# Kernel optimization log

Hardware: AMD Instinct MI355X
Metric: run time of the kernel (lower is better)

Reference implementation:

```python
import jax, jax.numpy as jnp
import numpy as np

B, T, H, C = 32, 2048, 1024, 1024

def setup_inputs() -> dict:
    key = jax.random.key(0)
    k1, k2, k3, k4, k5, k6 = jax.random.split(key, 6)
    decoder_output = jax.random.normal(k1, (B, 1, H), dtype=jnp.float32)
    encoder_outputs = jax.random.normal(k2, (B, T, H), dtype=jnp.float32)
    scale = 1.0 / np.sqrt(H)
    W = jax.random.normal(k3, (H, C), dtype=jnp.float32) * scale
    V = jax.random.normal(k4, (H, C), dtype=jnp.float32) * scale
    b = jax.random.uniform(k5, (C,), dtype=jnp.float32, minval=-0.1, maxval=0.1)
    w = jax.random.normal(k6, (C, 1), dtype=jnp.float32) * (1.0 / np.sqrt(C))
    return {"decoder_output": decoder_output, "encoder_outputs": encoder_outputs,
            "W": W, "V": V, "b": b, "w": w}

def reference(decoder_output, encoder_outputs, W, V, b, w):
    # Additive (Bahdanau) content attention.
    dec_proj = jnp.einsum('bqh,hc->bqc', decoder_output, W)   # [B,1,C]
    enc_proj = jnp.einsum('bth,hc->btc', encoder_outputs, V)  # [B,T,C]
    energy = jnp.tanh(dec_proj + enc_proj + b)                # [B,T,C]
    scores = jnp.einsum('btc,c->bt', energy, w[:, 0])         # [B,T]
    alignment = jax.nn.softmax(scores, axis=-1)               # [B,T]
    context = jnp.einsum('bt,bth->bh', alignment, encoder_outputs)  # [B,H]
    return context
```

## Files before the change

### kernel.cpp

```cpp
#include <hip/hip_runtime.h>
#include <hip/hip_bf16.h>
#include <stdint.h>

#define Bn 32
#define Tn 2048
#define Hn 1024
#define Cn 1024

typedef short short8 __attribute__((ext_vector_type(8)));
typedef float floatx4 __attribute__((ext_vector_type(4)));

__device__ __forceinline__ unsigned int bf16_rne(float f) {
    union { float f; unsigned int u; } v; v.f = f;
    unsigned int u = v.u;
    return (u + 0x7fffu + ((u >> 16) & 1u)) >> 16;
}

__global__ void k_dbias(const float* __restrict__ dec, const float* __restrict__ W,
                        const float* __restrict__ bias, float* __restrict__ dbias) {
    const int b  = blockIdx.x;
    const int c  = blockIdx.y * 256 + threadIdx.x;
    const int h0 = blockIdx.z * 256;
    const float* dv = dec + b * Hn + h0;
    const float* wp = W + (size_t)h0 * Cn + c;
    float acc = 0.f;
#pragma unroll 8
    for (int h = 0; h < 256; ++h)
        acc += dv[h] * wp[(size_t)h * Cn];
    if (blockIdx.z == 0) acc += bias[c];
    atomicAdd(&dbias[b * Cn + c], acc);
}

__global__ void k_vpack(const float* __restrict__ V, uint4* __restrict__ vp) {
    const int bid  = blockIdx.x;
    const int nt   = bid >> 5;
    const int kt   = bid & 31;
    const int lane = threadIdx.x;
    const int c    = nt * 16 + (lane & 15);
    const int k0   = kt * 32 + (lane >> 4) * 8;
    unsigned int h[8];
#pragma unroll
    for (int j = 0; j < 8; ++j)
        h[j] = bf16_rne(V[(size_t)(k0 + j) * Cn + c]);
    uint4 u;
    u.x = h[0] | (h[1] << 16);
    u.y = h[2] | (h[3] << 16);
    u.z = h[4] | (h[5] << 16);
    u.w = h[6] | (h[7] << 16);
    vp[(size_t)bid * 64 + lane] = u;
}

#define BLK_M 64
#define LDA   1032

struct ScoresShared {
    unsigned short A[BLK_M * LDA];
    float scores[BLK_M];
};

__global__ __launch_bounds__(512, 2)
void k_scores(const float* __restrict__ enc, const uint4* __restrict__ vp,
              const float* __restrict__ dbias, const float* __restrict__ wv,
              float* __restrict__ scores_g) {
    __shared__ ScoresShared sh;
    const int wg   = blockIdx.x;
    const int tid  = threadIdx.x;
    const int lane = tid & 63;
    const int wave = tid >> 6;
    const int b    = wg >> 5;
    const int row0 = wg * BLK_M;
    const int lhi  = lane >> 4;
    const int llo  = lane & 15;

    if (tid < BLK_M) sh.scores[tid] = 0.f;

    {
        const float4* ep = (const float4*)(enc + (size_t)row0 * Hn);
#pragma unroll 4
        for (int it = 0; it < 32; ++it) {
            int idx = tid + it * 512;
            int r   = idx >> 8;
            int c4  = idx & 255;
            float4 f = ep[r * 256 + c4];
            uint2 p;
            p.x = bf16_rne(f.x) | (bf16_rne(f.y) << 16);
            p.y = bf16_rne(f.z) | (bf16_rne(f.w) << 16);
            *(uint2*)&sh.A[r * LDA + c4 * 4] = p;
        }
    }
    __syncthreads();

    float score_part[16];
#pragma unroll
    for (int i = 0; i < 16; ++i) score_part[i] = 0.f;

    for (int ni = 0; ni < 2; ++ni) {
        const int colbase = (ni * 8 + wave) * 64;
        const int nt0     = colbase >> 4;

        floatx4 acc[4][4];
#pragma unroll
        for (int i = 0; i < 4; ++i)
#pragma unroll
            for (int j = 0; j < 4; ++j)
                acc[i][j] = (floatx4){0.f, 0.f, 0.f, 0.f};

#pragma unroll 2
        for (int kt = 0; kt < 32; ++kt) {
            short8 afr[4], bfr[4];
#pragma unroll
            for (int rg = 0; rg < 4; ++rg) {
                const unsigned short* ap = &sh.A[(rg * 16 + llo) * LDA + kt * 32 + lhi * 8];
                afr[rg] = *(const short8*)ap;
            }
#pragma unroll
            for (int j = 0; j < 4; ++j) {
                uint4 u = vp[((nt0 + j) * 32 + kt) * 64 + lane];
                bfr[j] = __builtin_bit_cast(short8, u);
            }
#pragma unroll
            for (int rg = 0; rg < 4; ++rg)
#pragma unroll
                for (int j = 0; j < 4; ++j)
                    acc[rg][j] = __builtin_amdgcn_mfma_f32_16x16x32_bf16(
                        afr[rg], bfr[j], acc[rg][j], 0, 0, 0);
        }

#pragma unroll
        for (int j = 0; j < 4; ++j) {
            const int c  = colbase + j * 16 + llo;
            const float db = dbias[b * Cn + c];
            const float wc = wv[c];
#pragma unroll
            for (int rg = 0; rg < 4; ++rg) {
#pragma unroll
                for (int r = 0; r < 4; ++r) {
                    float x = acc[rg][j][r] + db;
                    x = fminf(fmaxf(x, -12.f), 12.f);
                    float e = __expf(2.f * x);
                    float t = 1.f - 2.f / (e + 1.f);
                    score_part[rg * 4 + r] += t * wc;
                }
            }
        }
    }

#pragma unroll
    for (int i = 0; i < 16; ++i) {
        float v = score_part[i];
        v += __shfl_xor(v, 1);
        v += __shfl_xor(v, 2);
        v += __shfl_xor(v, 4);
        v += __shfl_xor(v, 8);
        score_part[i] = v;
    }
    if (llo == 0) {
#pragma unroll
        for (int rg = 0; rg < 4; ++rg)
#pragma unroll
            for (int r = 0; r < 4; ++r)
                atomicAdd(&sh.scores[rg * 16 + lhi * 4 + r], score_part[rg * 4 + r]);
    }
    __syncthreads();
    if (tid < BLK_M) scores_g[row0 + tid] = sh.scores[tid];
}

__global__ void k_softmax(const float* __restrict__ scores, float* __restrict__ align) {
    const int b   = blockIdx.x;
    const int tid = threadIdx.x;
    const float* s = scores + b * Tn;
    float v[8];
    float lmax = -1e30f;
#pragma unroll
    for (int i = 0; i < 8; ++i) { v[i] = s[tid + i * 256]; lmax = fmaxf(lmax, v[i]); }
    for (int off = 1; off < 64; off <<= 1) lmax = fmaxf(lmax, __shfl_xor(lmax, off));
    __shared__ float red[4];
    __shared__ float red2[4];
    if ((tid & 63) == 0) red[tid >> 6] = lmax;
    __syncthreads();
    lmax = fmaxf(fmaxf(red[0], red[1]), fmaxf(red[2], red[3]));
    float lsum = 0.f;
#pragma unroll
    for (int i = 0; i < 8; ++i) { v[i] = __expf(v[i] - lmax); lsum += v[i]; }
    for (int off = 1; off < 64; off <<= 1) lsum += __shfl_xor(lsum, off);
    if ((tid & 63) == 0) red2[tid >> 6] = lsum;
    __syncthreads();
    lsum = red2[0] + red2[1] + red2[2] + red2[3];
    const float inv = 1.f / lsum;
#pragma unroll
    for (int i = 0; i < 8; ++i) align[b * Tn + tid + i * 256] = v[i] * inv;
}

__global__ void k_context(const float* __restrict__ enc, const float* __restrict__ align,
                          float* __restrict__ out) {
    const int b   = blockIdx.x;
    const int tc  = blockIdx.y;
    const int tid = threadIdx.x;
    const float4* ep = (const float4*)(enc + ((size_t)b * Tn + tc * 256) * Hn);
    const float*  al = align + b * Tn + tc * 256;
    float4 acc = {0.f, 0.f, 0.f, 0.f};
    for (int t = 0; t < 256; ++t) {
        const float a = al[t];
        const float4 e = ep[t * 256 + tid];
        acc.x += a * e.x; acc.y += a * e.y; acc.z += a * e.z; acc.w += a * e.w;
    }
    float* op = out + b * Hn + tid * 4;
    atomicAdd(op + 0, acc.x);
    atomicAdd(op + 1, acc.y);
    atomicAdd(op + 2, acc.z);
    atomicAdd(op + 3, acc.w);
}

extern "C" void kernel_launch(void* const* d_in, const int* in_sizes, int n_in,
                              void* d_out, int out_size, void* d_ws, size_t ws_size,
                              hipStream_t stream) {
    const float* dec  = (const float*)d_in[0];
    const float* enc  = (const float*)d_in[1];
    const float* W    = (const float*)d_in[2];
    const float* V    = (const float*)d_in[3];
    const float* bias = (const float*)d_in[4];
    const float* wv   = (const float*)d_in[5];
    float* out = (float*)d_out;

    char* ws = (char*)d_ws;
    float* dbias  = (float*)(ws);
    uint4* vpack  = (uint4*)(ws + 131072);
    float* scores = (float*)(ws + 131072 + 2097152);
    float* align  = (float*)(ws + 131072 + 2097152 + 262144);

    hipMemsetAsync(dbias, 0, 131072, stream);
    hipMemsetAsync(d_out, 0, Bn * Cn * sizeof(float), stream);

    k_dbias  <<<dim3(32, 4, 4), 256, 0, stream>>>(dec, W, bias, dbias);
    k_vpack  <<<2048, 64, 0, stream>>>(V, vpack);
    k_scores <<<1024, 512, 0, stream>>>(enc, vpack, dbias, wv, scores);
    k_softmax<<<32, 256, 0, stream>>>(scores, align);
    k_context<<<dim3(32, 8), 256, 0, stream>>>(enc, align, out);
}
```

Before: 569.5 us.

## Pipeline encoder tile loads via direct-to-LDS copies and split context into partial-reduce kernels

The scores kernel now streams the fp32 encoder tile into shared memory in four K-chunks, double-buffered with global_load_lds, and converts it to bf16 at fragment-load time. It also computes both N halves in one K pass, prefetching the packed V fragments one step ahead. This is meant to overlap global loads with MFMA work, at the cost of more registers and larger LDS traffic, since fp32 is stored instead of bf16. The context kernel is split into a 32-way T-partitioned partial pass with more parallelism and a separate reduction kernel, replacing atomics and the output memset.

```diff
diff --git a/kernel.cpp b/kernel.cpp
--- a/kernel.cpp
+++ b/kernel.cpp
@@ -14,6 +14,17 @@
     union { float f; unsigned int u; } v; v.f = f;
     unsigned int u = v.u;
     return (u + 0x7fffu + ((u >> 16) & 1u)) >> 16;
+}
+
+__device__ __forceinline__ unsigned int pk_bf16(float a, float b) {
+    return bf16_rne(a) | (bf16_rne(b) << 16);
+}
+
+__device__ __forceinline__ void load_lds_16(const float* g, float* l) {
+    __builtin_amdgcn_global_load_lds(
+        (const __attribute__((address_space(1))) unsigned int*)g,
+        (__attribute__((address_space(3))) unsigned int*)l,
+        16, 0, 0);
 }
 
 __global__ void k_dbias(const float* __restrict__ dec, const float* __restrict__ W,
@@ -51,10 +62,12 @@
 }
 
 #define BLK_M 64
-#define LDA   1032
+#define KC    256
+#define NCH   4
+#define LDAF  260
 
 struct ScoresShared {
-    unsigned short A[BLK_M * LDA];
+    float A[2][BLK_M][LDAF];
     float scores[BLK_M];
 };
 
@@ -63,10 +76,10 @@
               const float* __restrict__ dbias, const float* __restrict__ wv,
               float* __restrict__ scores_g) {
     __shared__ ScoresShared sh;
-    const int wg   = blockIdx.x;
     const int tid  = threadIdx.x;
     const int lane = tid & 63;
-    const int wave = tid >> 6;
+    const int wid  = tid >> 6;
+    const int wg   = blockIdx.x;
     const int b    = wg >> 5;
     const int row0 = wg * BLK_M;
     const int lhi  = lane >> 4;
@@ -74,68 +87,105 @@
 
     if (tid < BLK_M) sh.scores[tid] = 0.f;
 
-    {
-        const float4* ep = (const float4*)(enc + (size_t)row0 * Hn);
-#pragma unroll 4
-        for (int it = 0; it < 32; ++it) {
-            int idx = tid + it * 512;
-            int r   = idx >> 8;
-            int c4  = idx & 255;
-            float4 f = ep[r * 256 + c4];
-            uint2 p;
-            p.x = bf16_rne(f.x) | (bf16_rne(f.y) << 16);
-            p.y = bf16_rne(f.z) | (bf16_rne(f.w) << 16);
-            *(uint2*)&sh.A[r * LDA + c4 * 4] = p;
+    const float* grow = enc + (size_t)row0 * Hn + lane * 4;
+
+#pragma unroll
+    for (int i = 0; i < 8; ++i) {
+        const int r = wid * 8 + i;
+        load_lds_16(grow + (size_t)r * Hn, &sh.A[0][r][0]);
+    }
+    __syncthreads();
+
+    const int nt0 = wid * 4;
+    const int nt1 = (wid + 8) * 4;
+
+    floatx4 acc[2][4][4];
+#pragma unroll
+    for (int n = 0; n < 2; ++n)
+#pragma unroll
+        for (int i = 0; i < 4; ++i)
+#pragma unroll
+            for (int j = 0; j < 4; ++j)
+                acc[n][i][j] = (floatx4){0.f, 0.f, 0.f, 0.f};
+
+    for (int c = 0; c < NCH; ++c) {
+        const int cb = c & 1;
+        const int kbase = c * 8;
+
+        uint4 bcur[8];
+#pragma unroll
+        for (int j = 0; j < 4; ++j) {
+            bcur[j]     = vp[((nt0 + j) * 32 + kbase) * 64 + lane];
+            bcur[4 + j] = vp[((nt1 + j) * 32 + kbase) * 64 + lane];
         }
-    }
-    __syncthreads();
+
+#pragma unroll
+        for (int kt = 0; kt < 8; ++kt) {
+            uint4 bnxt[8];
+            if (kt < 7) {
+                const int kg = kbase + kt + 1;
+#pragma unroll
+                for (int j = 0; j < 4; ++j) {
+                    bnxt[j]     = vp[((nt0 + j) * 32 + kg) * 64 + lane];
+                    bnxt[4 + j] = vp[((nt1 + j) * 32 + kg) * 64 + lane];
+                }
+            }
+            if (c < NCH - 1 && kt < 4) {
+                const int r0 = wid * 8 + kt * 2;
+                const float* gsrc = grow + (size_t)(c + 1) * KC;
+                load_lds_16(gsrc + (size_t)r0 * Hn,       &sh.A[cb ^ 1][r0][0]);
+                load_lds_16(gsrc + (size_t)(r0 + 1) * Hn, &sh.A[cb ^ 1][r0 + 1][0]);
+            }
+
+            short8 afr[4];
+#pragma unroll
+            for (int rg = 0; rg < 4; ++rg) {
+                const float* ap = &sh.A[cb][rg * 16 + llo][kt * 32 + lhi * 8];
+                float4 f0 = *(const float4*)ap;
+                float4 f1 = *(const float4*)(ap + 4);
+                uint4 u;
+                u.x = pk_bf16(f0.x, f0.y);
+                u.y = pk_bf16(f0.z, f0.w);
+                u.z = pk_bf16(f1.x, f1.y);
+                u.w = pk_bf16(f1.z, f1.w);
+                afr[rg] = __builtin_bit_cast(short8, u);
+            }
+
+#pragma unroll
+            for (int rg = 0; rg < 4; ++rg)
+#pragma unroll
+                for (int j = 0; j < 4; ++j) {
+                    acc[0][rg][j] = __builtin_amdgcn_mfma_f32_16x16x32_bf16(
+                        afr[rg], __builtin_bit_cast(short8, bcur[j]), acc[0][rg][j], 0, 0, 0);
+                    acc[1][rg][j] = __builtin_amdgcn_mfma_f32_16x16x32_bf16(
+                        afr[rg], __builtin_bit_cast(short8, bcur[4 + j]), acc[1][rg][j], 0, 0, 0);
+                }
+
+            if (kt < 7) {
+#pragma unroll
+                for (int j = 0; j < 8; ++j) bcur[j] = bnxt[j];
+            }
+        }
+        __syncthreads();
+    }
 
     float score_part[16];
 #pragma unroll
     for (int i = 0; i < 16; ++i) score_part[i] = 0.f;
 
+#pragma unroll
     for (int ni = 0; ni < 2; ++ni) {
-        const int colbase = (ni * 8 + wave) * 64;
-        const int nt0     = colbase >> 4;
-
-        floatx4 acc[4][4];
-#pragma unroll
-        for (int i = 0; i < 4; ++i)
-#pragma unroll
-            for (int j = 0; j < 4; ++j)
-                acc[i][j] = (floatx4){0.f, 0.f, 0.f, 0.f};
-
-#pragma unroll 2
-        for (int kt = 0; kt < 32; ++kt) {
-            short8 afr[4], bfr[4];
+        const int colbase = (ni * 8 + wid) * 64;
+#pragma unroll
+        for (int j = 0; j < 4; ++j) {
+            const int cc   = colbase + j * 16 + llo;
+            const float db = dbias[b * Cn + cc];
+            const float wc = wv[cc];
 #pragma unroll
             for (int rg = 0; rg < 4; ++rg) {
-                const unsigned short* ap = &sh.A[(rg * 16 + llo) * LDA + kt * 32 + lhi * 8];
-                afr[rg] = *(const short8*)ap;
-            }
-#pragma unroll
-            for (int j = 0; j < 4; ++j) {
-                uint4 u = vp[((nt0 + j) * 32 + kt) * 64 + lane];
-                bfr[j] = __builtin_bit_cast(short8, u);
-            }
-#pragma unroll
-            for (int rg = 0; rg < 4; ++rg)
-#pragma unroll
-                for (int j = 0; j < 4; ++j)
-                    acc[rg][j] = __builtin_amdgcn_mfma_f32_16x16x32_bf16(
-                        afr[rg], bfr[j], acc[rg][j], 0, 0, 0);
-        }
-
-#pragma unroll
-        for (int j = 0; j < 4; ++j) {
-            const int c  = colbase + j * 16 + llo;
-            const float db = dbias[b * Cn + c];
-            const float wc = wv[c];
-#pragma unroll
-            for (int rg = 0; rg < 4; ++rg) {
 #pragma unroll
                 for (int r = 0; r < 4; ++r) {
-                    float x = acc[rg][j][r] + db;
+                    float x = acc[ni][rg][j][r] + db;
                     x = fminf(fmaxf(x, -12.f), 12.f);
                     float e = __expf(2.f * x);
                     float t = 1.f - 2.f / (e + 1.f);
@@ -191,24 +241,32 @@
     for (int i = 0; i < 8; ++i) align[b * Tn + tid + i * 256] = v[i] * inv;
 }
 
-__global__ void k_context(const float* __restrict__ enc, const float* __restrict__ align,
-                          float* __restrict__ out) {
+__global__ void k_ctx_part(const float* __restrict__ enc, const float* __restrict__ align,
+                           float* __restrict__ part) {
     const int b   = blockIdx.x;
     const int tc  = blockIdx.y;
     const int tid = threadIdx.x;
-    const float4* ep = (const float4*)(enc + ((size_t)b * Tn + tc * 256) * Hn);
-    const float*  al = align + b * Tn + tc * 256;
-    float4 acc = {0.f, 0.f, 0.f, 0.f};
-    for (int t = 0; t < 256; ++t) {
-        const float a = al[t];
-        const float4 e = ep[t * 256 + tid];
-        acc.x += a * e.x; acc.y += a * e.y; acc.z += a * e.z; acc.w += a * e.w;
-    }
-    float* op = out + b * Hn + tid * 4;
-    atomicAdd(op + 0, acc.x);
-    atomicAdd(op + 1, acc.y);
-    atomicAdd(op + 2, acc.z);
-    atomicAdd(op + 3, acc.w);
+    const floatx4* ep = (const floatx4*)(enc + ((size_t)b * Tn + tc * 64) * Hn);
+    const float*   al = align + b * Tn + tc * 64;
+    floatx4 a0 = {0.f,0.f,0.f,0.f}, a1 = a0, a2 = a0, a3 = a0;
+    for (int t = 0; t < 64; t += 4) {
+        const float w0 = al[t], w1 = al[t+1], w2 = al[t+2], w3 = al[t+3];
+        a0 += w0 * ep[(t+0) * 256 + tid];
+        a1 += w1 * ep[(t+1) * 256 + tid];
+        a2 += w2 * ep[(t+2) * 256 + tid];
+        a3 += w3 * ep[(t+3) * 256 + tid];
+    }
+    ((floatx4*)part)[(tc * Bn + b) * 256 + tid] = (a0 + a1) + (a2 + a3);
+}
+
+__global__ void k_ctx_red(const float* __restrict__ part, float* __restrict__ out) {
+    const int idx = blockIdx.x * 256 + threadIdx.x;
+    const floatx4* p = (const floatx4*)part;
+    floatx4 s = {0.f,0.f,0.f,0.f};
+#pragma unroll
+    for (int tc = 0; tc < 32; ++tc)
+        s += p[tc * 8192 + idx];
+    ((floatx4*)out)[idx] = s;
 }
 
 extern "C" void kernel_launch(void* const* d_in, const int* in_sizes, int n_in,
@@ -226,14 +284,15 @@
     float* dbias  = (float*)(ws);
     uint4* vpack  = (uint4*)(ws + 131072);
     float* scores = (float*)(ws + 131072 + 2097152);
-    float* align  = (float*)(ws + 131072 + 2097152 + 262144);
-
-    hipMemsetAsync(dbias, 0, 131072, stream);
-    hipMemsetAsync(d_out, 0, Bn * Cn * sizeof(float), stream);
-
-    k_dbias  <<<dim3(32, 4, 4), 256, 0, stream>>>(dec, W, bias, dbias);
-    k_vpack  <<<2048, 64, 0, stream>>>(V, vpack);
-    k_scores <<<1024, 512, 0, stream>>>(enc, vpack, dbias, wv, scores);
-    k_softmax<<<32, 256, 0, stream>>>(scores, align);
-    k_context<<<dim3(32, 8), 256, 0, stream>>>(enc, align, out);
-}
+    float* align  = (float*)(ws + 2490368);
+    float* cpart  = (float*)(ws + 2752512);
+
+    (void)hipMemsetAsync(dbias, 0, 131072, stream);
+
+    k_dbias   <<<dim3(32, 4, 4), 256, 0, stream>>>(dec, W, bias, dbias);
+    k_vpack   <<<2048, 64, 0, stream>>>(V, vpack);
+    k_scores  <<<1024, 512, 0, stream>>>(enc, vpack, dbias, wv, scores);
+    k_softmax <<<32, 256, 0, stream>>>(scores, align);
+    k_ctx_part<<<dim3(32, 32), 256, 0, stream>>>(enc, align, cpart);
+    k_ctx_red <<<32, 256, 0, stream>>>(cpart, out);
+}
```

Result: slower. 821.4 us (+44.2%).
